# Kernel tuning notes

Measured on AMD Instinct MI355X. Metric: run time of the kernel, lower is better.

Reference implementation:

```python
import jax, jax.numpy as jnp
import numpy as np

B, S, C, L = 4, 32, 256, 512
H = 8
D = L // H  # head_size = 64
EPS = 1e-5


def _layernorm(x, g, b):
    mu = jnp.mean(x, axis=-1, keepdims=True)
    var = jnp.var(x, axis=-1, keepdims=True)
    return (x - mu) * jax.lax.rsqrt(var + EPS) * g + b


def setup_inputs() -> dict:
    key = jax.random.key(0)
    ks = jax.random.split(key, 12)
    s = 1.0 / np.sqrt(L)
    return {
        "x": jax.random.normal(ks[0], (B, S, C, L), dtype=jnp.float32),
        # per-head QKV weights, stacked: [H, D, L] (torch Linear(L, D, bias=False).weight)
        "Wq": jax.random.normal(ks[1], (H, D, L), dtype=jnp.float32) * s,
        "Wk": jax.random.normal(ks[2], (H, D, L), dtype=jnp.float32) * s,
        "Wv": jax.random.normal(ks[3], (H, D, L), dtype=jnp.float32) * s,
        # output projection Linear(L, L)
        "Wo": jax.random.normal(ks[4], (L, L), dtype=jnp.float32) * s,
        "bo": jnp.zeros((L,), dtype=jnp.float32),
        # FFN Linear(L, 4L) -> ReLU -> Linear(4L, L)
        "W1": jax.random.normal(ks[5], (4 * L, L), dtype=jnp.float32) * s,
        "b1": jnp.zeros((4 * L,), dtype=jnp.float32),
        "W2": jax.random.normal(ks[6], (L, 4 * L), dtype=jnp.float32) * (1.0 / np.sqrt(4 * L)),
        "b2": jnp.zeros((L,), dtype=jnp.float32),
        # LayerNorm params
        "g1": jnp.ones((L,), dtype=jnp.float32),
        "be1": jnp.zeros((L,), dtype=jnp.float32),
        "g2": jnp.ones((L,), dtype=jnp.float32),
        "be2": jnp.zeros((L,), dtype=jnp.float32),
    }


def reference(x, Wq, Wk, Wv, Wo, bo, W1, b1, W2, b2, g1, be1, g2, be2):
    # --- regional multi-head self-attention (pre-LN, residual) ---
    h = _layernorm(x, g1, be1)                        # [B,S,C,L]
    q = jnp.einsum('bscl,hdl->bhscd', h, Wq)          # [B,H,S,C,D]
    k = jnp.einsum('bscl,hdl->bhscd', h, Wk)
    v = jnp.einsum('bscl,hdl->bhscd', h, Wv)
    wei = jnp.einsum('bhsqd,bhskd->bhsqk', q, k) * (D ** -0.5)  # [B,H,S,C,C]
    wei = jax.nn.softmax(wei, axis=-1)                # no causal mask (tril unused)
    out = jnp.einsum('bhsqk,bhskd->bhsqd', wei, v)    # [B,H,S,C,D]
    out = jnp.transpose(out, (0, 2, 3, 1, 4)).reshape(x.shape[0], x.shape[1], x.shape[2], H * D)
    out = out @ Wo.T + bo                             # proj Linear(L, L)
    x = x + out
    # --- feed-forward (pre-LN, residual) ---
    h2 = _layernorm(x, g2, be2)
    ff = jax.nn.relu(h2 @ W1.T + b1) @ W2.T + b2      # [B,S,C,L]
    return x + ff
```

## Files before the change

### kernel.cpp

```cpp
#include <hip/hip_runtime.h>
#include <cstdint>
#include <cstddef>

#define NTOK 32768
#define LDIM 512
#define HN 8
#define HD 64
#define CC 256
#define FFD 2048

typedef __bf16 bf16x8 __attribute__((ext_vector_type(8)));
typedef float f32x4 __attribute__((ext_vector_type(4)));
typedef unsigned short u16;
typedef unsigned int u32;

__device__ __forceinline__ u16 f2bf(float f) {
  u32 u = __float_as_uint(f);
  u32 r = (u + 0x7fffu + ((u >> 16) & 1u)) >> 16;
  return (u16)r;
}

__device__ __forceinline__ void gload_lds16(const void* g, void* l) {
  __builtin_amdgcn_global_load_lds(
      (__attribute__((address_space(1))) void*)(void*)g,
      (__attribute__((address_space(3))) void*)l, 16, 0, 0);
}

__global__ void k_convall(const float* __restrict__ Wq, const float* __restrict__ Wk,
                          const float* __restrict__ Wv, const float* __restrict__ Wo,
                          const float* __restrict__ W1, const float* __restrict__ W2,
                          u16* __restrict__ wqkv, u16* __restrict__ wo,
                          u16* __restrict__ w1, u16* __restrict__ w2) {
  const int NW = 262144;
  const int MW = 1048576;
  const int TOT = 4 * NW + 2 * MW;
  int i = blockIdx.x * blockDim.x + threadIdx.x;
  const int st = gridDim.x * blockDim.x;
  for (; i < TOT; i += st) {
    if (i < NW) wqkv[i] = f2bf(Wq[i]);
    else if (i < 2 * NW) wqkv[i] = f2bf(Wk[i - NW]);
    else if (i < 3 * NW) wqkv[i] = f2bf(Wv[i - 2 * NW]);
    else if (i < 4 * NW) wo[i - 3 * NW] = f2bf(Wo[i - 3 * NW]);
    else if (i < 4 * NW + MW) w1[i - 4 * NW] = f2bf(W1[i - 4 * NW]);
    else w2[i - 4 * NW - MW] = f2bf(W2[i - 4 * NW - MW]);
  }
}

__global__ __launch_bounds__(256) void k_ln(const float* __restrict__ x,
                                            const float* __restrict__ gam,
                                            const float* __restrict__ bet,
                                            u16* __restrict__ out) {
  const int row = blockIdx.x * 4 + (threadIdx.x >> 6);
  const int lane = threadIdx.x & 63;
  const float4* xr = (const float4*)(x + (size_t)row * LDIM);
  float4 a = xr[lane * 2], b = xr[lane * 2 + 1];
  float s = a.x + a.y + a.z + a.w + b.x + b.y + b.z + b.w;
  float q = a.x * a.x + a.y * a.y + a.z * a.z + a.w * a.w +
            b.x * b.x + b.y * b.y + b.z * b.z + b.w * b.w;
#pragma unroll
  for (int m = 1; m < 64; m <<= 1) { s += __shfl_xor(s, m); q += __shfl_xor(q, m); }
  const float mean = s * (1.f / LDIM);
  const float rs = rsqrtf(q * (1.f / LDIM) - mean * mean + 1e-5f);
  const int c0 = lane * 8;
  const float4* g4 = (const float4*)(gam + c0);
  const float4* b4 = (const float4*)(bet + c0);
  float4 ga = g4[0], gb = g4[1], ba = b4[0], bb = b4[1];
  float vin[8] = {a.x, a.y, a.z, a.w, b.x, b.y, b.z, b.w};
  float vg[8]  = {ga.x, ga.y, ga.z, ga.w, gb.x, gb.y, gb.z, gb.w};
  float vb[8]  = {ba.x, ba.y, ba.z, ba.w, bb.x, bb.y, bb.z, bb.w};
  u16 o[8];
#pragma unroll
  for (int i = 0; i < 8; ++i) o[i] = f2bf((vin[i] - mean) * rs * vg[i] + vb[i]);
  *(bf16x8*)(out + (size_t)row * LDIM + c0) = *(bf16x8*)o;
}


__device__ __forceinline__ void stage_tile128(const u16* __restrict__ Ag,
                                              const u16* __restrict__ Bg, int K, int k0,
                                              u16* __restrict__ SA, u16* __restrict__ SB,
                                              int t) {
#pragma unroll
  for (int i = 0; i < 4; ++i) {
    const int p = i * 256 + t;
    const int r = p >> 3;
    const int c = ((p & 7) ^ (r & 7)) << 3;
    const int dst = (i * 256 + (t & ~63)) << 3;
    gload_lds16(Ag + (size_t)r * K + k0 + c, SA + dst);
    gload_lds16(Bg + (size_t)r * K + k0 + c, SB + dst);
  }
}

__device__ __forceinline__ bf16x8 ldsfrag64(const u16* __restrict__ s, int R, int ck) {
  return *(const bf16x8*)(s + R * 64 + ((ck ^ (R & 7)) << 3));
}

#define VM0 asm volatile("s_waitcnt vmcnt(0)" ::: "memory")
#define BARRIER asm volatile("s_barrier" ::: "memory")

template <int EPI>
__global__ __launch_bounds__(256, 2) void k_gemm128(const u16* __restrict__ A,
                                                    const u16* __restrict__ Bw, int K,
                                                    const float* __restrict__ bias,
                                                    const float* __restrict__ resid,
                                                    void* __restrict__ outp, int ldc,
                                                    int bmN) {
  extern __shared__ u16 lds_g[];
  const int t = threadIdx.x;
  const int lane = t & 63;
  const int w = t >> 6;
  const int wm = w >> 1, wn = w & 1;
  const int rl = lane & 15;
  const int kq = lane >> 4;
  const int nwg = gridDim.x;
  const int cpx = nwg >> 3;
  const int id = blockIdx.x;
  const int sid = (id & 7) * cpx + (id >> 3);
  const int bm = sid % bmN, bn = sid / bmN;

  const u16* Ag = A + (size_t)bm * 128 * K;
  const u16* Bg = Bw + (size_t)bn * 128 * K;

  f32x4 acc[4][4] = {};

  stage_tile128(Ag, Bg, K, 0, lds_g, lds_g + 16384, t);
  VM0;
  BARRIER;

  const int NT = K >> 6;
  for (int T = 0; T < NT; ++T) {
    const int par = T & 1, nx = par ^ 1;
    if (T + 1 < NT)
      stage_tile128(Ag, Bg, K, (T + 1) << 6, lds_g + nx * 8192,
                    lds_g + 16384 + nx * 8192, t);
    const u16* sA = lds_g + par * 8192;
    const u16* sB = lds_g + 16384 + par * 8192;
    bf16x8 a[4][2], b[4][2];
#pragma unroll
    for (int f = 0; f < 4; ++f)
#pragma unroll
      for (int kk = 0; kk < 2; ++kk) {
        a[f][kk] = ldsfrag64(sA, wm * 64 + f * 16 + rl, kk * 4 + kq);
        b[f][kk] = ldsfrag64(sB, wn * 64 + f * 16 + rl, kk * 4 + kq);
      }
#pragma unroll
    for (int f = 0; f < 4; ++f)
#pragma unroll
      for (int n = 0; n < 4; ++n) {
        acc[f][n] = __builtin_amdgcn_mfma_f32_16x16x32_bf16(a[f][0], b[n][0], acc[f][n], 0, 0, 0);
        acc[f][n] = __builtin_amdgcn_mfma_f32_16x16x32_bf16(a[f][1], b[n][1], acc[f][n], 0, 0, 0);
      }
    VM0;
    BARRIER;
  }

  const int rg = (lane >> 4) * 4;
  const int cl = lane & 15;
#pragma unroll
  for (int mi = 0; mi < 4; ++mi)
#pragma unroll
    for (int n = 0; n < 4; ++n) {
      const int mg = bm * 128 + wm * 64 + mi * 16 + rg;
      const int og = bn * 128 + wn * 64 + n * 16 + cl;
#pragma unroll
      for (int r = 0; r < 4; ++r) {
        float v = acc[mi][n][r];
        size_t idx = (size_t)(mg + r) * ldc + og;
        if (EPI == 0) {
          ((u16*)outp)[idx] = f2bf(v);
        } else if (EPI == 1) {
          ((float*)outp)[idx] = resid[idx] + v + bias[og];
        } else if (EPI == 2) {
          ((u16*)outp)[idx] = f2bf(fmaxf(v + bias[og], 0.f));
        } else {
          ((float*)outp)[idx] = ((float*)outp)[idx] + v + bias[og];
        }
      }
    }
}

__device__ __forceinline__ int swz(int row, int col) {
  return row * 64 + (col ^ ((row & 7) << 3));
}

__global__ __launch_bounds__(256) void k_attn(const u16* __restrict__ qkv,
                                              u16* __restrict__ attn) {
  __shared__ u16 Ks[64 * 64];
  __shared__ u16 Vt[64 * 64];
  __shared__ u16 Pl[4 * 64 * 64];
  const int t = threadIdx.x, lane = t & 63, w = t >> 6;
  const int region = blockIdx.x >> 3;
  const int h = blockIdx.x & 7;
  const size_t n0 = (size_t)region * CC;
  const int qb = w * 64;
  const int rl = lane & 15;
  const int kg = (lane >> 4) * 8;
  u16* Pw = Pl + w * 4096;

  bf16x8 aq[4][2];
#pragma unroll
  for (int f = 0; f < 4; ++f)
#pragma unroll
    for (int ks = 0; ks < 2; ++ks)
      aq[f][ks] = *(const bf16x8*)&qkv[(n0 + qb + f * 16 + rl) * 1536 + h * 64 + ks * 32 + kg];

  f32x4 oacc[4][4] = {};
  float mrun[4][4], lrun[4][4];
#pragma unroll
  for (int i = 0; i < 4; ++i)
#pragma unroll
    for (int j = 0; j < 4; ++j) { mrun[i][j] = -1e30f; lrun[i][j] = 0.f; }

  const int sr = t >> 2;
  const int sc = (t & 3) * 16;
  for (int kt = 0; kt < 4; ++kt) {
    if (kt) __syncthreads();
    {
      const u16* kp = &qkv[(n0 + kt * 64 + sr) * 1536 + 512 + h * 64 + sc];
      bf16x8 k0 = *(const bf16x8*)kp;
      bf16x8 k1 = *(const bf16x8*)(kp + 8);
      *(bf16x8*)&Ks[swz(sr, sc)] = k0;
      *(bf16x8*)&Ks[swz(sr, sc + 8)] = k1;
      const u16* vp = &qkv[(n0 + kt * 64 + sr) * 1536 + 1024 + h * 64 + sc];
      bf16x8 v0 = *(const bf16x8*)vp;
      bf16x8 v1 = *(const bf16x8*)(vp + 8);
#pragma unroll
      for (int i = 0; i < 8; ++i) Vt[swz(sc + i, sr)] = ((u16*)&v0)[i];
#pragma unroll
      for (int i = 0; i < 8; ++i) Vt[swz(sc + 8 + i, sr)] = ((u16*)&v1)[i];
    }
    __syncthreads();
    f32x4 sacc[4][4] = {};
#pragma unroll
    for (int ks = 0; ks < 2; ++ks) {
      bf16x8 bk[4];
#pragma unroll
      for (int f = 0; f < 4; ++f) bk[f] = *(const bf16x8*)&Ks[swz(f * 16 + rl, ks * 32 + kg)];
#pragma unroll
      for (int i = 0; i < 4; ++i)
#pragma unroll
        for (int j = 0; j < 4; ++j)
          sacc[i][j] = __builtin_amdgcn_mfma_f32_16x16x32_bf16(aq[i][ks], bk[j], sacc[i][j], 0, 0, 0);
    }
#pragma unroll
    for (int i = 0; i < 4; ++i)
#pragma unroll
      for (int j = 0; j < 4; ++j)
#pragma unroll
        for (int r = 0; r < 4; ++r) sacc[i][j][r] *= 0.125f;
#pragma unroll
    for (int i = 0; i < 4; ++i) {
#pragma unroll
      for (int r = 0; r < 4; ++r) {
        float v = fmaxf(fmaxf(sacc[i][0][r], sacc[i][1][r]), fmaxf(sacc[i][2][r], sacc[i][3][r]));
#pragma unroll
        for (int m = 1; m < 16; m <<= 1) v = fmaxf(v, __shfl_xor(v, m));
        float mnew = fmaxf(mrun[i][r], v);
        float fac = __expf(mrun[i][r] - mnew);
        mrun[i][r] = mnew;
        float ps = 0.f;
#pragma unroll
        for (int fn = 0; fn < 4; ++fn) {
          float p = __expf(sacc[i][fn][r] - mnew);
          sacc[i][fn][r] = p;
          ps += p;
        }
#pragma unroll
        for (int m = 1; m < 16; m <<= 1) ps += __shfl_xor(ps, m);
        lrun[i][r] = lrun[i][r] * fac + ps;
#pragma unroll
        for (int fd = 0; fd < 4; ++fd) oacc[i][fd][r] *= fac;
      }
#pragma unroll
      for (int fn = 0; fn < 4; ++fn)
#pragma unroll
        for (int r = 0; r < 4; ++r)
          Pw[swz(i * 16 + (lane >> 4) * 4 + r, fn * 16 + rl)] = f2bf(sacc[i][fn][r]);
    }
#pragma unroll
    for (int ks = 0; ks < 2; ++ks) {
      bf16x8 ap[4], bv[4];
#pragma unroll
      for (int f = 0; f < 4; ++f) ap[f] = *(const bf16x8*)&Pw[swz(f * 16 + rl, ks * 32 + kg)];
#pragma unroll
      for (int f = 0; f < 4; ++f) bv[f] = *(const bf16x8*)&Vt[swz(f * 16 + rl, ks * 32 + kg)];
#pragma unroll
      for (int i = 0; i < 4; ++i)
#pragma unroll
        for (int j = 0; j < 4; ++j)
          oacc[i][j] = __builtin_amdgcn_mfma_f32_16x16x32_bf16(ap[i], bv[j], oacc[i][j], 0, 0, 0);
    }
  }
#pragma unroll
  for (int i = 0; i < 4; ++i)
#pragma unroll
    for (int fd = 0; fd < 4; ++fd)
#pragma unroll
      for (int r = 0; r < 4; ++r) {
        float v = oacc[i][fd][r] / lrun[i][r];
        attn[(n0 + qb + i * 16 + (lane >> 4) * 4 + r) * 512 + h * 64 + fd * 16 + rl] = f2bf(v);
      }
}

extern "C" void kernel_launch(void* const* d_in, const int* in_sizes, int n_in,
                              void* d_out, int out_size, void* d_ws, size_t ws_size,
                              hipStream_t stream) {
  (void)in_sizes; (void)n_in; (void)out_size; (void)ws_size;
  const float* x   = (const float*)d_in[0];
  const float* Wq  = (const float*)d_in[1];
  const float* Wk  = (const float*)d_in[2];
  const float* Wv  = (const float*)d_in[3];
  const float* Wo  = (const float*)d_in[4];
  const float* bo  = (const float*)d_in[5];
  const float* W1  = (const float*)d_in[6];
  const float* b1  = (const float*)d_in[7];
  const float* W2  = (const float*)d_in[8];
  const float* b2  = (const float*)d_in[9];
  const float* g1  = (const float*)d_in[10];
  const float* be1 = (const float*)d_in[11];
  const float* g2  = (const float*)d_in[12];
  const float* be2 = (const float*)d_in[13];
  float* out = (float*)d_out;

  char* ws = (char*)d_ws;
  u16* wqkv = (u16*)(ws + 0);
  u16* wo   = (u16*)(ws + 1572864);
  u16* w1   = (u16*)(ws + 2097152);
  u16* w2   = (u16*)(ws + 4194304);
  u16* regA = (u16*)(ws + 6291456);
  u16* regB = (u16*)(ws + 39845888);

  const size_t LDSB = 65536;

  k_convall<<<1024, 256, 0, stream>>>(Wq, Wk, Wv, Wo, W1, W2, wqkv, wo, w1, w2);
  k_ln<<<NTOK / 4, 256, 0, stream>>>(x, g1, be1, regA);
  k_gemm128<0><<<dim3(256 * 12), 256, LDSB, stream>>>(regA, wqkv, 512, nullptr, nullptr, regB, 1536, 256);
  k_attn<<<dim3(4 * 32 * 8), 256, 0, stream>>>(regB, regA);
  k_gemm128<1><<<dim3(256 * 4), 256, LDSB, stream>>>(regA, wo, 512, bo, x, out, 512, 256);
  k_ln<<<NTOK / 4, 256, 0, stream>>>(out, g2, be2, regA);
  k_gemm128<2><<<dim3(256 * 16), 256, LDSB, stream>>>(regA, w1, 512, b1, nullptr, regB, 2048, 256);
  k_gemm128<3><<<dim3(256 * 4), 256, LDSB, stream>>>(regB, w2, 2048, b2, nullptr, out, 512, 256);
}
```

Measured before the change: 510.6 us.

## Widen GEMM tiles to 128x256 with 8 waves and K-step of 32

New measurement: 1.660 ms. +225.1%, slower.

```diff
diff --git a/kernel.cpp b/kernel.cpp
--- a/kernel.cpp
+++ b/kernel.cpp
@@ -75,40 +75,43 @@
 }
 
 
-__device__ __forceinline__ void stage_tile128(const u16* __restrict__ Ag,
-                                              const u16* __restrict__ Bg, int K, int k0,
-                                              u16* __restrict__ SA, u16* __restrict__ SB,
-                                              int t) {
-#pragma unroll
-  for (int i = 0; i < 4; ++i) {
-    const int p = i * 256 + t;
-    const int r = p >> 3;
-    const int c = ((p & 7) ^ (r & 7)) << 3;
-    const int dst = (i * 256 + (t & ~63)) << 3;
-    gload_lds16(Ag + (size_t)r * K + k0 + c, SA + dst);
-    gload_lds16(Bg + (size_t)r * K + k0 + c, SB + dst);
-  }
-}
-
-__device__ __forceinline__ bf16x8 ldsfrag64(const u16* __restrict__ s, int R, int ck) {
-  return *(const bf16x8*)(s + R * 64 + ((ck ^ (R & 7)) << 3));
+__device__ __forceinline__ void stage_tile(const u16* __restrict__ Ag,
+                                           const u16* __restrict__ Bg, int K, int k0,
+                                           u16* __restrict__ SA, u16* __restrict__ SB,
+                                           int t) {
+  {
+    const int r = t >> 2;
+    const int c = ((t & 3) ^ ((r >> 1) & 3)) << 3;
+    gload_lds16(Ag + (size_t)r * K + k0 + c, SA + ((t & ~63) << 3));
+  }
+#pragma unroll
+  for (int i = 0; i < 2; ++i) {
+    const int p = i * 512 + t;
+    const int r = p >> 2;
+    const int c = ((p & 3) ^ ((r >> 1) & 3)) << 3;
+    gload_lds16(Bg + (size_t)r * K + k0 + c, SB + ((i * 512 + (t & ~63)) << 3));
+  }
+}
+
+__device__ __forceinline__ bf16x8 ldsfrag32(const u16* __restrict__ s, int R, int kq) {
+  return *(const bf16x8*)(s + R * 32 + ((kq ^ ((R >> 1) & 3)) << 3));
 }
 
 #define VM0 asm volatile("s_waitcnt vmcnt(0)" ::: "memory")
 #define BARRIER asm volatile("s_barrier" ::: "memory")
 
 template <int EPI>
-__global__ __launch_bounds__(256, 2) void k_gemm128(const u16* __restrict__ A,
-                                                    const u16* __restrict__ Bw, int K,
-                                                    const float* __restrict__ bias,
-                                                    const float* __restrict__ resid,
-                                                    void* __restrict__ outp, int ldc,
-                                                    int bmN) {
+__global__ __launch_bounds__(512, 6) void k_gemm(const u16* __restrict__ A,
+                                                 const u16* __restrict__ Bw, int K,
+                                                 const float* __restrict__ bias,
+                                                 const float* __restrict__ resid,
+                                                 void* __restrict__ outp, int ldc,
+                                                 int bmN) {
   extern __shared__ u16 lds_g[];
   const int t = threadIdx.x;
   const int lane = t & 63;
   const int w = t >> 6;
-  const int wm = w >> 1, wn = w & 1;
+  const int wm = w >> 2, wn = w & 3;
   const int rl = lane & 15;
   const int kq = lane >> 4;
   const int nwg = gridDim.x;
@@ -118,37 +121,32 @@
   const int bm = sid % bmN, bn = sid / bmN;
 
   const u16* Ag = A + (size_t)bm * 128 * K;
-  const u16* Bg = Bw + (size_t)bn * 128 * K;
+  const u16* Bg = Bw + (size_t)bn * 256 * K;
 
   f32x4 acc[4][4] = {};
 
-  stage_tile128(Ag, Bg, K, 0, lds_g, lds_g + 16384, t);
+  stage_tile(Ag, Bg, K, 0, lds_g, lds_g + 8192, t);
   VM0;
   BARRIER;
 
-  const int NT = K >> 6;
+  const int NT = K >> 5;
   for (int T = 0; T < NT; ++T) {
     const int par = T & 1, nx = par ^ 1;
     if (T + 1 < NT)
-      stage_tile128(Ag, Bg, K, (T + 1) << 6, lds_g + nx * 8192,
-                    lds_g + 16384 + nx * 8192, t);
-    const u16* sA = lds_g + par * 8192;
-    const u16* sB = lds_g + 16384 + par * 8192;
-    bf16x8 a[4][2], b[4][2];
+      stage_tile(Ag, Bg, K, (T + 1) << 5, lds_g + nx * 4096,
+                 lds_g + 8192 + nx * 8192, t);
+    const u16* sA = lds_g + par * 4096;
+    const u16* sB = lds_g + 8192 + par * 8192;
+    bf16x8 a[4], b[4];
+#pragma unroll
+    for (int f = 0; f < 4; ++f) a[f] = ldsfrag32(sA, wm * 64 + f * 16 + rl, kq);
+#pragma unroll
+    for (int n = 0; n < 4; ++n) b[n] = ldsfrag32(sB, wn * 64 + n * 16 + rl, kq);
 #pragma unroll
     for (int f = 0; f < 4; ++f)
 #pragma unroll
-      for (int kk = 0; kk < 2; ++kk) {
-        a[f][kk] = ldsfrag64(sA, wm * 64 + f * 16 + rl, kk * 4 + kq);
-        b[f][kk] = ldsfrag64(sB, wn * 64 + f * 16 + rl, kk * 4 + kq);
-      }
-#pragma unroll
-    for (int f = 0; f < 4; ++f)
-#pragma unroll
-      for (int n = 0; n < 4; ++n) {
-        acc[f][n] = __builtin_amdgcn_mfma_f32_16x16x32_bf16(a[f][0], b[n][0], acc[f][n], 0, 0, 0);
-        acc[f][n] = __builtin_amdgcn_mfma_f32_16x16x32_bf16(a[f][1], b[n][1], acc[f][n], 0, 0, 0);
-      }
+      for (int n = 0; n < 4; ++n)
+        acc[f][n] = __builtin_amdgcn_mfma_f32_16x16x32_bf16(a[f], b[n], acc[f][n], 0, 0, 0);
     VM0;
     BARRIER;
   }
@@ -160,7 +158,7 @@
 #pragma unroll
     for (int n = 0; n < 4; ++n) {
       const int mg = bm * 128 + wm * 64 + mi * 16 + rg;
-      const int og = bn * 128 + wn * 64 + n * 16 + cl;
+      const int og = bn * 256 + wn * 64 + n * 16 + cl;
 #pragma unroll
       for (int r = 0; r < 4; ++r) {
         float v = acc[mi][n][r];
@@ -329,14 +327,14 @@
   u16* regA = (u16*)(ws + 6291456);
   u16* regB = (u16*)(ws + 39845888);
 
-  const size_t LDSB = 65536;
+  const size_t LDSB = 49152;
 
   k_convall<<<1024, 256, 0, stream>>>(Wq, Wk, Wv, Wo, W1, W2, wqkv, wo, w1, w2);
   k_ln<<<NTOK / 4, 256, 0, stream>>>(x, g1, be1, regA);
-  k_gemm128<0><<<dim3(256 * 12), 256, LDSB, stream>>>(regA, wqkv, 512, nullptr, nullptr, regB, 1536, 256);
+  k_gemm<0><<<dim3(256 * 6), 512, LDSB, stream>>>(regA, wqkv, 512, nullptr, nullptr, regB, 1536, 256);
   k_attn<<<dim3(4 * 32 * 8), 256, 0, stream>>>(regB, regA);
-  k_gemm128<1><<<dim3(256 * 4), 256, LDSB, stream>>>(regA, wo, 512, bo, x, out, 512, 256);
+  k_gemm<1><<<dim3(256 * 2), 512, LDSB, stream>>>(regA, wo, 512, bo, x, out, 512, 256);
   k_ln<<<NTOK / 4, 256, 0, stream>>>(out, g2, be2, regA);
-  k_gemm128<2><<<dim3(256 * 16), 256, LDSB, stream>>>(regA, w1, 512, b1, nullptr, regB, 2048, 256);
-  k_gemm128<3><<<dim3(256 * 4), 256, LDSB, stream>>>(regB, w2, 2048, b2, nullptr, out, 512, 256);
-}
+  k_gemm<2><<<dim3(256 * 8), 512, LDSB, stream>>>(regA, w1, 512, b1, nullptr, regB, 2048, 256);
+  k_gemm<3><<<dim3(256 * 2), 512, LDSB, stream>>>(regB, w2, 2048, b2, nullptr, out, 512, 256);
+}
```
